# Optimization experiments

Measured on AMD Instinct MI355X. Metric: run time of the kernel, lower is better.

Reference implementation:

```python
import jax, jax.numpy as jnp
import numpy as np

B, CIN, COUT, K = 4096, 128, 128, 9  # batch, in_ch, out_ch, board size / n_offsets


def setup_inputs() -> dict:
    key = jax.random.key(0)
    k1, k2, k3 = jax.random.split(key, 3)
    inputs = jax.random.normal(k1, (B, CIN, K, K), dtype=jnp.float32)   # [B, Cin, 9, 9]
    weights = jax.random.normal(k2, (K, COUT, CIN), dtype=jnp.float32)  # per-offset linear
    bias = jax.random.normal(k3, (K, COUT), dtype=jnp.float32)
    return {"inputs": inputs, "weights": weights, "bias": bias}


def reference(inputs, weights, bias):
    # For each vertical offset k (row of the 9x9 board), gather the slice
    # inputs[:, :, k, :] and apply the k-th linear map plus its bias.
    # out[b, k, oc, x] = sum_i W[k, oc, i] * inputs[b, i, k, x] + bias[k, oc]
    out = jnp.einsum('bikx,koi->bkox', inputs, weights)  # [B, 9, Cout, 9]
    out = out + bias[None, :, :, None]
    return out
```

## Files before the change

kernel.cpp:

```cpp
#include <hip/hip_runtime.h>
#include <hip/hip_bf16.h>


#define NB   4096
#define CINC 128
#define COUTC 128
#define NK   9
#define NX   9
#define BT   16
#define NCOL (BT * NX)
#define LDK  136

typedef __attribute__((ext_vector_type(8))) short short8;
typedef __attribute__((ext_vector_type(4))) float floatx4;

__device__ __forceinline__ short f2bf(float f) {
    union { float f; unsigned u; } v; v.f = f;
    unsigned r = v.u + 0x7fff + ((v.u >> 16) & 1);
    return (short)(r >> 16);
}

__global__ __launch_bounds__(512, 4) void GatherVertical_40656160424516_kernel(
    const float* __restrict__ in, const float* __restrict__ w,
    const float* __restrict__ bias, float* __restrict__ out)
{
    __shared__ short Wl[COUTC * LDK];
    __shared__ short Il[NCOL * LDK];

    const int t = threadIdx.x;
    const int k = blockIdx.x % NK;
    const int btile = blockIdx.x / NK;
    const int b0 = btile * BT;

    const float* wk = w + k * (COUTC * CINC);
    #pragma unroll
    for (int it = 0; it < 8; ++it) {
        int idx4 = it * 512 + t;
        int flat = idx4 * 4;
        int oc = flat >> 7;
        int i  = flat & 127;
        float4 v = *(const float4*)(wk + flat);
        short4 s;
        s.x = f2bf(v.x); s.y = f2bf(v.y); s.z = f2bf(v.z); s.w = f2bf(v.w);
        *(short4*)&Wl[oc * LDK + i] = s;
    }

    const float* inb = in + (size_t)b0 * (CINC * NK * NX) + k * NX;
    #pragma unroll
    for (int it = 0; it < 36; ++it) {
        int f = it * 512 + t;
        int bl = f / (CINC * NX);
        int rem = f - bl * (CINC * NX);
        int i = rem / NX;
        int x = rem - i * NX;
        float v = inb[bl * (CINC * NK * NX) + i * (NK * NX) + x];
        Il[(bl * NX + x) * LDK + i] = f2bf(v);
    }

    __syncthreads();

    const int lane = t & 63;
    const int wv = t >> 6;
    const int lc = lane & 15;
    const int quad = lane >> 4;

    floatx4 acc[9];
    #pragma unroll
    for (int n = 0; n < 9; ++n) acc[n] = (floatx4){0.f, 0.f, 0.f, 0.f};

    const int oc_base = wv * 16;
    #pragma unroll
    for (int s = 0; s < 4; ++s) {
        int kof = s * 32 + quad * 8;
        short8 a = *(const short8*)&Wl[(oc_base + lc) * LDK + kof];
        #pragma unroll
        for (int n = 0; n < 9; ++n) {
            short8 bfr = *(const short8*)&Il[(n * 16 + lc) * LDK + kof];
            acc[n] = __builtin_amdgcn_mfma_f32_16x16x32_bf16(a, bfr, acc[n], 0, 0, 0);
        }
    }

    const float* bk = bias + k * COUTC;
    float bsv[4];
    #pragma unroll
    for (int r = 0; r < 4; ++r) bsv[r] = bk[oc_base + quad * 4 + r];

    #pragma unroll
    for (int n = 0; n < 9; ++n) {
        int nx = n * 16 + lc;
        int bl = nx / 9;
        int x = nx - bl * 9;
        float* op = out + (size_t)(b0 + bl) * (NK * COUTC * NX) + k * (COUTC * NX)
                        + (oc_base + quad * 4) * NX + x;
        #pragma unroll
        for (int r = 0; r < 4; ++r)
            op[r * NX] = acc[n][r] + bsv[r];
    }
}

extern "C" void kernel_launch(void* const* d_in, const int* in_sizes, int n_in,
                              void* d_out, int out_size, void* d_ws, size_t ws_size,
                              hipStream_t stream) {
    const float* in  = (const float*)d_in[0];
    const float* w   = (const float*)d_in[1];
    const float* bs  = (const float*)d_in[2];
    float* out = (float*)d_out;
    dim3 grid((NB / BT) * NK);
    dim3 block(512);
    GatherVertical_40656160424516_kernel<<<grid, block, 0, stream>>>(in, w, bs, out);
}
```

Measured before the change: 353.4 us.

## Load weight fragments directly to registers and remap blocks across XCDs

Each wave now loads its A-fragments of the weight matrix straight from global memory into registers, converting to bf16 there. This drops the weight shared-memory tile and one LDS round trip. The smaller shared footprint lets launch bounds request 6 blocks per CU instead of 4. Block indices are remapped so the 9 k-offsets of one batch tile land on the same XCD, which should improve L2 reuse of input rows. In exchange, global loads of weights become less coalesced (each lane reads 32 bytes with a row stride), and register pressure rises.

```diff
diff --git a/kernel.cpp b/kernel.cpp
--- a/kernel.cpp
+++ b/kernel.cpp
@@ -20,30 +20,45 @@
     return (short)(r >> 16);
 }
 
-__global__ __launch_bounds__(512, 4) void GatherVertical_40656160424516_kernel(
+__global__ __launch_bounds__(512, 6) void GatherVertical_40656160424516_kernel(
     const float* __restrict__ in, const float* __restrict__ w,
     const float* __restrict__ bias, float* __restrict__ out)
 {
-    __shared__ short Wl[COUTC * LDK];
     __shared__ short Il[NCOL * LDK];
 
     const int t = threadIdx.x;
-    const int k = blockIdx.x % NK;
-    const int btile = blockIdx.x / NK;
+
+    const int j = blockIdx.x;
+    const int xcd = j & 7;
+    const int slot = j >> 3;
+    const int grp = slot / 9;
+    const int k = slot - grp * 9;
+    const int btile = grp * 8 + xcd;
     const int b0 = btile * BT;
 
+    const int lane = t & 63;
+    const int wv = t >> 6;
+    const int lc = lane & 15;
+    const int quad = lane >> 4;
+    const int oc_base = wv * 16;
+
     const float* wk = w + k * (COUTC * CINC);
+    short8 afr[4];
     #pragma unroll
-    for (int it = 0; it < 8; ++it) {
-        int idx4 = it * 512 + t;
-        int flat = idx4 * 4;
-        int oc = flat >> 7;
-        int i  = flat & 127;
-        float4 v = *(const float4*)(wk + flat);
-        short4 s;
-        s.x = f2bf(v.x); s.y = f2bf(v.y); s.z = f2bf(v.z); s.w = f2bf(v.w);
-        *(short4*)&Wl[oc * LDK + i] = s;
+    for (int s = 0; s < 4; ++s) {
+        const float* wp = wk + (oc_base + lc) * CINC + s * 32 + quad * 8;
+        float4 w0 = *(const float4*)wp;
+        float4 w1 = *(const float4*)(wp + 4);
+        short8 a;
+        a[0] = f2bf(w0.x); a[1] = f2bf(w0.y); a[2] = f2bf(w0.z); a[3] = f2bf(w0.w);
+        a[4] = f2bf(w1.x); a[5] = f2bf(w1.y); a[6] = f2bf(w1.z); a[7] = f2bf(w1.w);
+        afr[s] = a;
     }
+
+    const float* bk = bias + k * COUTC;
+    float bsv[4];
+    #pragma unroll
+    for (int r = 0; r < 4; ++r) bsv[r] = bk[oc_base + quad * 4 + r];
 
     const float* inb = in + (size_t)b0 * (CINC * NK * NX) + k * NX;
     #pragma unroll
@@ -59,31 +74,19 @@
 
     __syncthreads();
 
-    const int lane = t & 63;
-    const int wv = t >> 6;
-    const int lc = lane & 15;
-    const int quad = lane >> 4;
-
     floatx4 acc[9];
     #pragma unroll
     for (int n = 0; n < 9; ++n) acc[n] = (floatx4){0.f, 0.f, 0.f, 0.f};
 
-    const int oc_base = wv * 16;
     #pragma unroll
     for (int s = 0; s < 4; ++s) {
         int kof = s * 32 + quad * 8;
-        short8 a = *(const short8*)&Wl[(oc_base + lc) * LDK + kof];
         #pragma unroll
         for (int n = 0; n < 9; ++n) {
             short8 bfr = *(const short8*)&Il[(n * 16 + lc) * LDK + kof];
-            acc[n] = __builtin_amdgcn_mfma_f32_16x16x32_bf16(a, bfr, acc[n], 0, 0, 0);
+            acc[n] = __builtin_amdgcn_mfma_f32_16x16x32_bf16(afr[s], bfr, acc[n], 0, 0, 0);
         }
     }
-
-    const float* bk = bias + k * COUTC;
-    float bsv[4];
-    #pragma unroll
-    for (int r = 0; r < 4; ++r) bsv[r] = bk[oc_base + quad * 4 + r];
 
     #pragma unroll
     for (int n = 0; n < 9; ++n) {
```

After: 352.7 us. Within noise of the previous version (-0.2%).
